# Performance work log

Measured on AMD Instinct MI355X. Metric: run time of the kernel, lower is better.

The kernel has to match this reference:

```python
import jax, jax.numpy as jnp
import numpy as np
import math

E, K = 8, 4
IN, OUT = 768, 768
B, S = 16, 512

def _nearest_factors(n):
    r = int(math.sqrt(n))
    while n % r != 0:
        r -= 1
    r = max(r, 1)
    return r, n // r

D1, D2 = _nearest_factors(IN)      # 24, 32
DO1, DO2 = _nearest_factors(OUT)   # 24, 32

def _cv_squared(v):
    v = v.astype(jnp.float32)
    return jnp.var(v, ddof=1) / (jnp.mean(v) ** 2 + 1e-10)

def setup_inputs() -> dict:
    key = jax.random.key(0)
    ks = jax.random.split(key, 8)
    eye = lambda d: jnp.broadcast_to(jnp.eye(d, dtype=jnp.float32), (E, d, d))
    return {
        "x": jax.random.normal(ks[0], (B, S, IN), jnp.float32),
        "w_gate": 0.02 * jax.random.normal(ks[1], (IN, E), jnp.float32),
        "weight": 0.02 * jax.random.normal(ks[2], (E, OUT, IN), jnp.float32),
        "res_weight": 0.02 * jax.random.normal(ks[3], (OUT, IN), jnp.float32),
        "curve1_in": eye(D1) + 0.01 * jax.random.normal(ks[4], (E, D1, D1), jnp.float32),
        "curve2_in": eye(D2) + 0.01 * jax.random.normal(ks[5], (E, D2, D2), jnp.float32),
        "curve1_out": eye(DO1) + 0.01 * jax.random.normal(ks[6], (E, DO1, DO1), jnp.float32),
        "curve2_out": eye(DO2) + 0.01 * jax.random.normal(ks[7], (E, DO2, DO2), jnp.float32),
    }

def reference(x, w_gate, weight, res_weight, curve1_in, curve2_in, curve1_out, curve2_out):
    b = x.shape[0]
    # ---- noisy_top_k_gating (eval mode: clean logits, no noise) ----
    xm = x.mean(-2)                         # [B, IN]
    logits = xm @ w_gate                    # [B, E]
    top_vals, top_idx = jax.lax.top_k(logits, min(K + 1, E))
    tk_vals = top_vals[:, :K]
    tk_idx = top_idx[:, :K]
    tk_gates = jax.nn.softmax(tk_vals, axis=1)
    gates = jnp.zeros_like(logits).at[jnp.arange(b)[:, None], tk_idx].set(tk_gates)
    load = (gates > 0).sum(0)               # eval: gates_to_load
    importance = gates.sum(0)
    loss = 0.01 * (_cv_squared(importance) + _cv_squared(load))
    # ---- curve-factor expert weight composition (k*2 >= n_experts branch) ----
    rtw = (weight - res_weight).reshape(E, DO1, DO2, D1, D2)
    rtw = jnp.einsum('bij,bjklm->biklm', curve1_out, rtw)
    rtw = jnp.einsum('bik,bjklm->bjilm', curve2_out, rtw)
    rtw = jnp.einsum('bil,bjklm->bjkim', curve1_in, rtw)
    rtw = jnp.einsum('bim,bjklm->bjkli', curve2_in, rtw)
    rtw = rtw.reshape(E, OUT, IN)
    # dropout p=0.1 is identity in eval mode
    expert_weights = res_weight + 0.9 * jnp.sum(rtw[None] * gates[:, :, None, None], axis=1)  # [B, OUT, IN]
    y = jnp.einsum('bsj,bkj->bsk', x, expert_weights)  # [B, S, OUT]
    return y, loss
```

## Files before the change

kernel.cpp:

```cpp
#include <hip/hip_runtime.h>
#include <hip/hip_bf16.h>

typedef unsigned short u16;
typedef __attribute__((ext_vector_type(8))) short bf16x8;
typedef __attribute__((ext_vector_type(4))) float f32x4;

#define NE 8
#define NTOPK 4
#define NIN 768
#define NOUT 768
#define NB 16
#define NS 512
#define YSZ (NB * NS * NOUT)
#define EWN (NOUT * NIN)

#define OFF_PART  0u
#define OFF_GATES 3145728u
#define OFF_XBF   3146240u
#define OFF_WD    15729152u
#define OFF_T1T   25166336u
#define OFF_RTW   34603520u
#define OFF_EW    44040704u

#define PRE_BAR(N) asm volatile("s_waitcnt vmcnt(" #N ")\n\ts_barrier" ::: "memory")
#define POST_BAR() asm volatile("s_waitcnt lgkmcnt(0)\n\ts_barrier" ::: "memory")

__device__ __forceinline__ u16 f2bf(float f) {
  union { float f; unsigned u; } v; v.f = f;
  unsigned r = v.u + 0x7fffu + ((v.u >> 16) & 1u);
  return (u16)(r >> 16);
}
__device__ __forceinline__ float bf2f(u16 h) {
  union { unsigned u; float f; } v; v.u = ((unsigned)h) << 16;
  return v.f;
}
__device__ __forceinline__ unsigned cvt2(float a, float b) {
  unsigned r;
  asm("v_cvt_pk_bf16_f32 %0, %1, %2" : "=v"(r) : "v"(a), "v"(b));
  return r;
}
__device__ __forceinline__ void gload16(const void* g, void* l) {
  __builtin_amdgcn_global_load_lds(
      (const __attribute__((address_space(1))) unsigned int*)g,
      (__attribute__((address_space(3))) unsigned int*)l, 16, 0, 0);
}
__device__ __forceinline__ void storeC(float* p, float v) { *p = v; }
__device__ __forceinline__ void storeC(u16* p, float v) { *p = f2bf(v); }

__global__ __launch_bounds__(256) void k_p0(const float* __restrict__ x,
                                            float* __restrict__ part,
                                            u16* __restrict__ xbf,
                                            const float* __restrict__ w,
                                            const float* __restrict__ res,
                                            u16* __restrict__ Wd) {
  int u = blockIdx.x;
  if (u < 1024) {
    int t = threadIdx.x;
    if (t < 192) {
      int b = u >> 6;
      int sc = u & 63;
      int c = t * 4;
      float a0 = 0.f, a1 = 0.f, a2 = 0.f, a3 = 0.f;
      int s0 = sc * 8;
#pragma unroll
      for (int r = 0; r < 8; ++r) {
        size_t ro = ((size_t)(b * NS + s0 + r)) * NIN;
        float4 v = *(const float4*)(x + ro + c);
        a0 += v.x; a1 += v.y; a2 += v.z; a3 += v.w;
        ushort4 o;
        o.x = f2bf(v.x); o.y = f2bf(v.y); o.z = f2bf(v.z); o.w = f2bf(v.w);
        *(ushort4*)(xbf + ro + c) = o;
      }
      float4 pv; pv.x = a0; pv.y = a1; pv.z = a2; pv.w = a3;
      *(float4*)(part + (size_t)(b * 64 + sc) * NIN + c) = pv;
    }
  } else {
    int b2 = u - 1024;
    int e = b2 / 288;
    int blk = b2 % 288;
    size_t base = (size_t)blk * 2048 + threadIdx.x * 8;
    float4 wa = *(const float4*)(w + (size_t)e * EWN + base);
    float4 wb = *(const float4*)(w + (size_t)e * EWN + base + 4);
    float4 ra = *(const float4*)(res + base);
    float4 rb = *(const float4*)(res + base + 4);
    bf16x8 o;
    o[0] = (short)f2bf(wa.x - ra.x); o[1] = (short)f2bf(wa.y - ra.y);
    o[2] = (short)f2bf(wa.z - ra.z); o[3] = (short)f2bf(wa.w - ra.w);
    o[4] = (short)f2bf(wb.x - rb.x); o[5] = (short)f2bf(wb.y - rb.y);
    o[6] = (short)f2bf(wb.z - rb.z); o[7] = (short)f2bf(wb.w - rb.w);
    *(bf16x8*)(Wd + (size_t)e * EWN + base) = o;
  }
}

__device__ __forceinline__ void body_logits(int b, float* red,
                                            const float* __restrict__ part,
                                            const float* __restrict__ w_gate,
                                            float* __restrict__ gates_out) {
  int tid = threadIdx.x;
  float p[NE] = {0.f, 0.f, 0.f, 0.f, 0.f, 0.f, 0.f, 0.f};
  for (int i = tid; i < NIN; i += 256) {
    float s = 0.f;
#pragma unroll
    for (int sc = 0; sc < 64; ++sc) s += part[(size_t)(b * 64 + sc) * NIN + i];
    float xmv = s * (1.0f / (float)NS);
#pragma unroll
    for (int e = 0; e < NE; ++e) p[e] += xmv * w_gate[i * NE + e];
  }
#pragma unroll
  for (int e = 0; e < NE; ++e) {
    float v = p[e];
    for (int off = 32; off; off >>= 1) v += __shfl_down(v, off);
    if ((tid & 63) == 0) red[(tid >> 6) * NE + e] = v;
  }
  __syncthreads();
  if (tid == 0) {
    float v[NE]; bool used[NE];
    for (int e = 0; e < NE; ++e) {
      v[e] = red[e] + red[NE + e] + red[2 * NE + e] + red[3 * NE + e];
      used[e] = false;
    }
    int idxs[NTOPK]; float vals[NTOPK];
    for (int t = 0; t < NTOPK; ++t) {
      int best = 0; float bv = -3.4e38f;
      for (int e = 0; e < NE; ++e)
        if (!used[e] && v[e] > bv) { bv = v[e]; best = e; }
      used[best] = true; idxs[t] = best; vals[t] = bv;
    }
    float m = vals[0];
    float ex[NTOPK]; float se = 0.f;
    for (int t = 0; t < NTOPK; ++t) { ex[t] = expf(vals[t] - m); se += ex[t]; }
    float g[NE];
    for (int e = 0; e < NE; ++e) g[e] = 0.f;
    for (int t = 0; t < NTOPK; ++t) g[idxs[t]] = ex[t] / se;
    for (int e = 0; e < NE; ++e) gates_out[b * NE + e] = g[e];
  }
}

__device__ __forceinline__ void body_kron(int bid, u16* lb,
                                          const float* __restrict__ c1,
                                          const float* __restrict__ c2,
                                          const u16* __restrict__ B,
                                          u16* __restrict__ C) {
  const int tid = threadIdx.x;
  const int lane = tid & 63;
  const int w = tid >> 6;
  const int wr = w >> 1, wc = w & 1;
  const int fr = lane & 15;
  const int kq = lane >> 4;
  const int swz = (bid & 7) * 72 + (bid >> 3);
  const int mb = swz % 12;
  const int nb = (swz / 12) % 6;
  const int e = swz / 72;
  const int m0 = mb * 64, n0 = nb * 128;
  const u16* Bb = B + (size_t)e * EWN;
  const float* c1b = c1 + e * 24 * 24;
  const float* c2b = c2 + e * 32 * 32;
  const int r1a = (m0 >> 5) + wr;
  float c2r[2][8];
  {
    const float* p0 = c2b + fr * 32 + kq * 8;
    const float* p1 = c2b + (16 + fr) * 32 + kq * 8;
#pragma unroll
    for (int j = 0; j < 8; ++j) { c2r[0][j] = p0[j]; c2r[1][j] = p1[j]; }
  }
  const int ob1 = (w * 2) * 1024 + lane * 16;
  const int ob2 = ob1 + 1024;
  const int rowB1 = ob1 >> 6, colB1 = ob1 & 63;
  const int rowB2 = ob2 >> 6, colB2 = ob2 & 63;

  auto STAGE = [&](int t) {
    int s = t & 3;
    int k0 = t * 32;
    gload16((const char*)Bb + ((size_t)(n0 + rowB1) * NIN + k0) * 2 + colB1,
            (char*)(lb + s * 4096) + ob1);
    gload16((const char*)Bb + ((size_t)(n0 + rowB2) * NIN + k0) * 2 + colB2,
            (char*)(lb + s * 4096) + ob2);
  };
  f32x4 acc[2][4] = {};
  auto COMPUTE = [&](int t) {
    int s = t & 3;
    const float ca = c1b[r1a * 24 + t];
    bf16x8 aF[2], bF[4];
#pragma unroll
    for (int m = 0; m < 2; ++m) {
      const float* cr = c2r[m];
      union { unsigned u[4]; bf16x8 v; } pk;
      pk.u[0] = cvt2(ca * cr[0], ca * cr[1]);
      pk.u[1] = cvt2(ca * cr[2], ca * cr[3]);
      pk.u[2] = cvt2(ca * cr[4], ca * cr[5]);
      pk.u[3] = cvt2(ca * cr[6], ca * cr[7]);
      aF[m] = pk.v;
    }
#pragma unroll
    for (int n = 0; n < 4; ++n)
      bF[n] = *(const bf16x8*)(lb + (size_t)s * 4096 + (wc * 64 + n * 16 + fr) * 32 + kq * 8);
#pragma unroll
    for (int m = 0; m < 2; ++m)
#pragma unroll
      for (int n = 0; n < 4; ++n)
        acc[m][n] = __builtin_amdgcn_mfma_f32_16x16x32_bf16(aF[m], bF[n], acc[m][n], 0, 0, 0);
  };

  STAGE(0); STAGE(1); STAGE(2); STAGE(3);
  for (int i = 0; i < 10; ++i) {
    PRE_BAR(4);
    COMPUTE(2 * i); COMPUTE(2 * i + 1);
    POST_BAR();
    STAGE(2 * i + 4); STAGE(2 * i + 5);
  }
  PRE_BAR(4);  COMPUTE(20); COMPUTE(21);  POST_BAR();
  PRE_BAR(0);  COMPUTE(22); COMPUTE(23);

  u16* Cb = C + (size_t)e * EWN;
#pragma unroll
  for (int m = 0; m < 2; ++m) {
    int rb = m0 + wr * 32 + m * 16 + kq * 4;
#pragma unroll
    for (int n = 0; n < 4; ++n) {
      int col = n0 + wc * 64 + n * 16 + fr;
#pragma unroll
      for (int r = 0; r < 4; ++r)
        storeC(Cb + (size_t)(rb + r) * NIN + col, acc[m][n][r]);
    }
  }
}

__global__ __launch_bounds__(256) void k_p1(const float* c1, const float* c2,
                                            const u16* B, u16* C,
                                            const float* part, const float* w_gate,
                                            float* gates) {
  __shared__ __attribute__((aligned(128))) u16 lB[4 * 128 * 32];
  __shared__ float red[NB * NE];
  if (blockIdx.x < 576) body_kron(blockIdx.x, lB, c1, c2, B, C);
  else                  body_logits(blockIdx.x - 576, red, part, w_gate, gates);
}
__global__ __launch_bounds__(256) void k_p2(const float* c1, const float* c2,
                                            const u16* B, u16* C) {
  __shared__ __attribute__((aligned(128))) u16 lB[4 * 128 * 32];
  body_kron(blockIdx.x, lB, c1, c2, B, C);
}

__global__ __launch_bounds__(256) void k_p3(const u16* __restrict__ rtwb,
                                            const float* __restrict__ res,
                                            const float* __restrict__ g,
                                            u16* __restrict__ ew,
                                            float* __restrict__ loss_out) {
  __shared__ float gsh[NB * NE];
  int bid = blockIdx.x;
  int tid = threadIdx.x;
  if (tid < NB * NE) gsh[tid] = 0.9f * g[tid];
  __syncthreads();
  if (bid == 0 && tid == 0) {
    float imp[NE], ld[NE];
    for (int e = 0; e < NE; ++e) {
      float si = 0.f, sl = 0.f;
      for (int b = 0; b < NB; ++b) {
        float gg = g[b * NE + e];
        si += gg; sl += (gg > 0.f) ? 1.f : 0.f;
      }
      imp[e] = si; ld[e] = sl;
    }
    float loss = 0.f;
    for (int which = 0; which < 2; ++which) {
      const float* a = which ? ld : imp;
      float mean = 0.f;
      for (int e = 0; e < NE; ++e) mean += a[e];
      mean *= (1.0f / NE);
      float var = 0.f;
      for (int e = 0; e < NE; ++e) { float d = a[e] - mean; var += d * d; }
      var *= (1.0f / (NE - 1));
      loss += var / (mean * mean + 1e-10f);
    }
    loss_out[0] = 0.01f * loss;
  }
  size_t base = ((size_t)bid * 256 + tid) * 8;
  float rv[NE][8];
#pragma unroll
  for (int e = 0; e < NE; ++e) {
    bf16x8 v = *(const bf16x8*)(rtwb + (size_t)e * EWN + base);
#pragma unroll
    for (int j = 0; j < 8; ++j) rv[e][j] = bf2f((u16)v[j]);
  }
  float r8[8];
  {
    float4 ra = *(const float4*)(res + base);
    float4 rb = *(const float4*)(res + base + 4);
    r8[0] = ra.x; r8[1] = ra.y; r8[2] = ra.z; r8[3] = ra.w;
    r8[4] = rb.x; r8[5] = rb.y; r8[6] = rb.z; r8[7] = rb.w;
  }
  for (int b = 0; b < NB; ++b) {
    float a[8];
#pragma unroll
    for (int j = 0; j < 8; ++j) a[j] = r8[j];
#pragma unroll
    for (int e = 0; e < NE; ++e) {
      float gg = gsh[b * NE + e];
#pragma unroll
      for (int j = 0; j < 8; ++j) a[j] += gg * rv[e][j];
    }
    bf16x8 o;
#pragma unroll
    for (int j = 0; j < 8; ++j) o[j] = (short)f2bf(a[j]);
    *(bf16x8*)(ew + (size_t)b * EWN + base) = o;
  }
}

__global__ __launch_bounds__(256) void k_main(const u16* __restrict__ A,
                                              const u16* __restrict__ Bw,
                                              float* __restrict__ C) {
  __shared__ __attribute__((aligned(128))) u16 la[3 * 128 * 32];
  __shared__ __attribute__((aligned(128))) u16 lb[3 * 128 * 32];
  const int tid = threadIdx.x;
  const int lane = tid & 63;
  const int w = tid >> 6;
  const int wr = w >> 1, wc = w & 1;
  const int fr = lane & 15;
  const int kq = lane >> 4;
  const int swz = (blockIdx.x & 7) * 48 + (blockIdx.x >> 3);
  const int mb = swz % 4;
  const int nb = (swz / 4) % 6;
  const int b = swz / 24;
  const int m0 = mb * 128, n0 = nb * 128;
  const u16* Ab = A + (size_t)b * NS * NIN;
  const u16* Bb = Bw + (size_t)b * EWN;
  const int ob1 = tid * 16;
  const int ob2 = ob1 + 4096;
  const int row1 = ob1 >> 6, col1 = ob1 & 63;
  const int row2 = ob2 >> 6, col2 = ob2 & 63;

  auto STAGE = [&](int t) {
    int s = t % 3;
    int k0 = t * 32;
    gload16((const char*)Ab + ((size_t)(m0 + row1) * NIN + k0) * 2 + col1,
            (char*)(la + s * 4096) + ob1);
    gload16((const char*)Ab + ((size_t)(m0 + row2) * NIN + k0) * 2 + col2,
            (char*)(la + s * 4096) + ob2);
    gload16((const char*)Bb + ((size_t)(n0 + row1) * NIN + k0) * 2 + col1,
            (char*)(lb + s * 4096) + ob1);
    gload16((const char*)Bb + ((size_t)(n0 + row2) * NIN + k0) * 2 + col2,
            (char*)(lb + s * 4096) + ob2);
  };
  f32x4 acc[4][4] = {};
  auto COMPUTE = [&](int t) {
    int s = t % 3;
    bf16x8 aF[4], bF[4];
#pragma unroll
    for (int m = 0; m < 4; ++m)
      aF[m] = *(const bf16x8*)(la + (size_t)s * 4096 + (wr * 64 + m * 16 + fr) * 32 + kq * 8);
#pragma unroll
    for (int n = 0; n < 4; ++n)
      bF[n] = *(const bf16x8*)(lb + (size_t)s * 4096 + (wc * 64 + n * 16 + fr) * 32 + kq * 8);
#pragma unroll
    for (int m = 0; m < 4; ++m)
#pragma unroll
      for (int n = 0; n < 4; ++n)
        acc[m][n] = __builtin_amdgcn_mfma_f32_16x16x32_bf16(aF[m], bF[n], acc[m][n], 0, 0, 0);
  };

  STAGE(0); STAGE(1); STAGE(2);
  for (int i = 0; i < 10; ++i) {
    PRE_BAR(4);
    COMPUTE(2 * i); COMPUTE(2 * i + 1);
    POST_BAR();
    STAGE(2 * i + 3); STAGE(2 * i + 4);
  }
  PRE_BAR(4);  COMPUTE(20); COMPUTE(21);  POST_BAR();
  STAGE(23);
  PRE_BAR(0);  COMPUTE(22); COMPUTE(23);

  float* Cb = C + (size_t)b * NS * NOUT;
#pragma unroll
  for (int m = 0; m < 4; ++m) {
    int rb = m0 + wr * 64 + m * 16 + kq * 4;
#pragma unroll
    for (int n = 0; n < 4; ++n) {
      int col = n0 + wc * 64 + n * 16 + fr;
#pragma unroll
      for (int r = 0; r < 4; ++r)
        Cb[(size_t)(rb + r) * NOUT + col] = acc[m][n][r];
    }
  }
}

extern "C" void kernel_launch(void* const* d_in, const int* in_sizes, int n_in,
                              void* d_out, int out_size, void* d_ws, size_t ws_size,
                              hipStream_t stream) {
  const float* x = (const float*)d_in[0];
  const float* w_gate = (const float*)d_in[1];
  const float* weight = (const float*)d_in[2];
  const float* res_w = (const float*)d_in[3];
  const float* c1i = (const float*)d_in[4];
  const float* c2i = (const float*)d_in[5];
  const float* c1o = (const float*)d_in[6];
  const float* c2o = (const float*)d_in[7];

  char* ws = (char*)d_ws;
  float* part = (float*)(ws + OFF_PART);
  float* gates = (float*)(ws + OFF_GATES);
  u16* xbf = (u16*)(ws + OFF_XBF);
  u16* Wd = (u16*)(ws + OFF_WD);
  u16* T1t = (u16*)(ws + OFF_T1T);
  u16* rtwb = (u16*)(ws + OFF_RTW);
  u16* ew = (u16*)(ws + OFF_EW);

  float* y = (float*)d_out;
  float* loss = y + YSZ;

  k_p0<<<dim3(3328), 256, 0, stream>>>(x, part, xbf, weight, res_w, Wd);
  k_p1<<<dim3(592), 256, 0, stream>>>(c1i, c2i, Wd, T1t, part, w_gate, gates);
  k_p2<<<dim3(576), 256, 0, stream>>>(c1o, c2o, T1t, rtwb);
  k_p3<<<dim3(288), 256, 0, stream>>>(rtwb, res_w, gates, ew, loss);
  k_main<<<dim3(384), 256, 0, stream>>>(xbf, ew, y);
}
```

Baseline: 76.37 us.

## Factor Kronecker curve transforms into separate small-mode contractions

Replaces the MFMA-based Kronecker GEMM, which multiplied each expert's 768x768 difference matrix by a dense 768x768 Kron(c1,c2) operand, with two separable scalar contractions: a 32x32 mode product (k_s1) followed by a 24x24 mode product (k_s2), each using LDS-cached factor matrices. The weight-minus-residual subtraction is fused into the first stage instead of running as its own pass. This cuts FLOPs substantially but drops tensor cores, adds two extra kernel launches, and round-trips a bf16 intermediate U through global memory, which adds another rounding step. The k_s2 reads are strided by 32*768, and k_s1 holds a per-thread 32-float register row.

```diff
diff --git a/kernel.cpp b/kernel.cpp
--- a/kernel.cpp
+++ b/kernel.cpp
@@ -17,7 +17,7 @@
 #define OFF_PART  0u
 #define OFF_GATES 3145728u
 #define OFF_XBF   3146240u
-#define OFF_WD    15729152u
+#define OFF_U     15729152u
 #define OFF_T1T   25166336u
 #define OFF_RTW   34603520u
 #define OFF_EW    44040704u
@@ -34,61 +34,34 @@
   union { unsigned u; float f; } v; v.u = ((unsigned)h) << 16;
   return v.f;
 }
-__device__ __forceinline__ unsigned cvt2(float a, float b) {
-  unsigned r;
-  asm("v_cvt_pk_bf16_f32 %0, %1, %2" : "=v"(r) : "v"(a), "v"(b));
-  return r;
-}
 __device__ __forceinline__ void gload16(const void* g, void* l) {
   __builtin_amdgcn_global_load_lds(
       (const __attribute__((address_space(1))) unsigned int*)g,
       (__attribute__((address_space(3))) unsigned int*)l, 16, 0, 0);
 }
-__device__ __forceinline__ void storeC(float* p, float v) { *p = v; }
-__device__ __forceinline__ void storeC(u16* p, float v) { *p = f2bf(v); }
-
-__global__ __launch_bounds__(256) void k_p0(const float* __restrict__ x,
-                                            float* __restrict__ part,
-                                            u16* __restrict__ xbf,
-                                            const float* __restrict__ w,
-                                            const float* __restrict__ res,
-                                            u16* __restrict__ Wd) {
+
+__global__ __launch_bounds__(256) void k_x(const float* __restrict__ x,
+                                           float* __restrict__ part,
+                                           u16* __restrict__ xbf) {
   int u = blockIdx.x;
-  if (u < 1024) {
-    int t = threadIdx.x;
-    if (t < 192) {
-      int b = u >> 6;
-      int sc = u & 63;
-      int c = t * 4;
-      float a0 = 0.f, a1 = 0.f, a2 = 0.f, a3 = 0.f;
-      int s0 = sc * 8;
-#pragma unroll
-      for (int r = 0; r < 8; ++r) {
-        size_t ro = ((size_t)(b * NS + s0 + r)) * NIN;
-        float4 v = *(const float4*)(x + ro + c);
-        a0 += v.x; a1 += v.y; a2 += v.z; a3 += v.w;
-        ushort4 o;
-        o.x = f2bf(v.x); o.y = f2bf(v.y); o.z = f2bf(v.z); o.w = f2bf(v.w);
-        *(ushort4*)(xbf + ro + c) = o;
-      }
-      float4 pv; pv.x = a0; pv.y = a1; pv.z = a2; pv.w = a3;
-      *(float4*)(part + (size_t)(b * 64 + sc) * NIN + c) = pv;
-    }
-  } else {
-    int b2 = u - 1024;
-    int e = b2 / 288;
-    int blk = b2 % 288;
-    size_t base = (size_t)blk * 2048 + threadIdx.x * 8;
-    float4 wa = *(const float4*)(w + (size_t)e * EWN + base);
-    float4 wb = *(const float4*)(w + (size_t)e * EWN + base + 4);
-    float4 ra = *(const float4*)(res + base);
-    float4 rb = *(const float4*)(res + base + 4);
-    bf16x8 o;
-    o[0] = (short)f2bf(wa.x - ra.x); o[1] = (short)f2bf(wa.y - ra.y);
-    o[2] = (short)f2bf(wa.z - ra.z); o[3] = (short)f2bf(wa.w - ra.w);
-    o[4] = (short)f2bf(wb.x - rb.x); o[5] = (short)f2bf(wb.y - rb.y);
-    o[6] = (short)f2bf(wb.z - rb.z); o[7] = (short)f2bf(wb.w - rb.w);
-    *(bf16x8*)(Wd + (size_t)e * EWN + base) = o;
+  int t = threadIdx.x;
+  if (t < 192) {
+    int b = u >> 6;
+    int sc = u & 63;
+    int c = t * 4;
+    float a0 = 0.f, a1 = 0.f, a2 = 0.f, a3 = 0.f;
+    int s0 = sc * 8;
+#pragma unroll
+    for (int r = 0; r < 8; ++r) {
+      size_t ro = ((size_t)(b * NS + s0 + r)) * NIN;
+      float4 v = *(const float4*)(x + ro + c);
+      a0 += v.x; a1 += v.y; a2 += v.z; a3 += v.w;
+      ushort4 o;
+      o.x = f2bf(v.x); o.y = f2bf(v.y); o.z = f2bf(v.z); o.w = f2bf(v.w);
+      *(ushort4*)(xbf + ro + c) = o;
+    }
+    float4 pv; pv.x = a0; pv.y = a1; pv.z = a2; pv.w = a3;
+    *(float4*)(part + (size_t)(b * 64 + sc) * NIN + c) = pv;
   }
 }
 
@@ -136,108 +109,78 @@
   }
 }
 
-__device__ __forceinline__ void body_kron(int bid, u16* lb,
-                                          const float* __restrict__ c1,
-                                          const float* __restrict__ c2,
-                                          const u16* __restrict__ B,
-                                          u16* __restrict__ C) {
-  const int tid = threadIdx.x;
-  const int lane = tid & 63;
-  const int w = tid >> 6;
-  const int wr = w >> 1, wc = w & 1;
-  const int fr = lane & 15;
-  const int kq = lane >> 4;
-  const int swz = (bid & 7) * 72 + (bid >> 3);
-  const int mb = swz % 12;
-  const int nb = (swz / 12) % 6;
-  const int e = swz / 72;
-  const int m0 = mb * 64, n0 = nb * 128;
-  const u16* Bb = B + (size_t)e * EWN;
-  const float* c1b = c1 + e * 24 * 24;
-  const float* c2b = c2 + e * 32 * 32;
-  const int r1a = (m0 >> 5) + wr;
-  float c2r[2][8];
-  {
-    const float* p0 = c2b + fr * 32 + kq * 8;
-    const float* p1 = c2b + (16 + fr) * 32 + kq * 8;
-#pragma unroll
-    for (int j = 0; j < 8; ++j) { c2r[0][j] = p0[j]; c2r[1][j] = p1[j]; }
-  }
-  const int ob1 = (w * 2) * 1024 + lane * 16;
-  const int ob2 = ob1 + 1024;
-  const int rowB1 = ob1 >> 6, colB1 = ob1 & 63;
-  const int rowB2 = ob2 >> 6, colB2 = ob2 & 63;
-
-  auto STAGE = [&](int t) {
-    int s = t & 3;
-    int k0 = t * 32;
-    gload16((const char*)Bb + ((size_t)(n0 + rowB1) * NIN + k0) * 2 + colB1,
-            (char*)(lb + s * 4096) + ob1);
-    gload16((const char*)Bb + ((size_t)(n0 + rowB2) * NIN + k0) * 2 + colB2,
-            (char*)(lb + s * 4096) + ob2);
-  };
-  f32x4 acc[2][4] = {};
-  auto COMPUTE = [&](int t) {
-    int s = t & 3;
-    const float ca = c1b[r1a * 24 + t];
-    bf16x8 aF[2], bF[4];
-#pragma unroll
-    for (int m = 0; m < 2; ++m) {
-      const float* cr = c2r[m];
-      union { unsigned u[4]; bf16x8 v; } pk;
-      pk.u[0] = cvt2(ca * cr[0], ca * cr[1]);
-      pk.u[1] = cvt2(ca * cr[2], ca * cr[3]);
-      pk.u[2] = cvt2(ca * cr[4], ca * cr[5]);
-      pk.u[3] = cvt2(ca * cr[6], ca * cr[7]);
-      aF[m] = pk.v;
-    }
-#pragma unroll
-    for (int n = 0; n < 4; ++n)
-      bF[n] = *(const bf16x8*)(lb + (size_t)s * 4096 + (wc * 64 + n * 16 + fr) * 32 + kq * 8);
-#pragma unroll
-    for (int m = 0; m < 2; ++m)
-#pragma unroll
-      for (int n = 0; n < 4; ++n)
-        acc[m][n] = __builtin_amdgcn_mfma_f32_16x16x32_bf16(aF[m], bF[n], acc[m][n], 0, 0, 0);
-  };
-
-  STAGE(0); STAGE(1); STAGE(2); STAGE(3);
-  for (int i = 0; i < 10; ++i) {
-    PRE_BAR(4);
-    COMPUTE(2 * i); COMPUTE(2 * i + 1);
-    POST_BAR();
-    STAGE(2 * i + 4); STAGE(2 * i + 5);
-  }
-  PRE_BAR(4);  COMPUTE(20); COMPUTE(21);  POST_BAR();
-  PRE_BAR(0);  COMPUTE(22); COMPUTE(23);
-
-  u16* Cb = C + (size_t)e * EWN;
-#pragma unroll
-  for (int m = 0; m < 2; ++m) {
-    int rb = m0 + wr * 32 + m * 16 + kq * 4;
-#pragma unroll
-    for (int n = 0; n < 4; ++n) {
-      int col = n0 + wc * 64 + n * 16 + fr;
-#pragma unroll
-      for (int r = 0; r < 4; ++r)
-        storeC(Cb + (size_t)(rb + r) * NIN + col, acc[m][n][r]);
-    }
-  }
-}
-
-__global__ __launch_bounds__(256) void k_p1(const float* c1, const float* c2,
-                                            const u16* B, u16* C,
-                                            const float* part, const float* w_gate,
-                                            float* gates) {
-  __shared__ __attribute__((aligned(128))) u16 lB[4 * 128 * 32];
+template <bool WSUB>
+__global__ __launch_bounds__(256) void k_s1(const float* __restrict__ wsrc,
+                                            const float* __restrict__ res,
+                                            const u16* __restrict__ tin,
+                                            const float* __restrict__ c2,
+                                            u16* __restrict__ U,
+                                            const float* __restrict__ part,
+                                            const float* __restrict__ w_gate,
+                                            float* __restrict__ gates) {
+  __shared__ float c2lds[32 * 32];
   __shared__ float red[NB * NE];
-  if (blockIdx.x < 576) body_kron(blockIdx.x, lB, c1, c2, B, C);
-  else                  body_logits(blockIdx.x - 576, red, part, w_gate, gates);
-}
-__global__ __launch_bounds__(256) void k_p2(const float* c1, const float* c2,
-                                            const u16* B, u16* C) {
-  __shared__ __attribute__((aligned(128))) u16 lB[4 * 128 * 32];
-  body_kron(blockIdx.x, lB, c1, c2, B, C);
+  int bid = blockIdx.x;
+  if (bid >= 576) {
+    if (gates) body_logits(bid - 576, red, part, w_gate, gates);
+    return;
+  }
+  int e = bid / 72, rem = bid % 72, l = rem / 3, chunk = rem % 3;
+  int jk = chunk * 256 + threadIdx.x;
+  for (int idx = threadIdx.x; idx < 1024; idx += 256) c2lds[idx] = c2[e * 1024 + idx];
+  __syncthreads();
+  float wr[32];
+  if (WSUB) {
+    const float* wp = wsrc + ((size_t)(e * NIN + jk)) * NIN + l * 32;
+    const float* rp = res + (size_t)jk * NIN + l * 32;
+#pragma unroll
+    for (int q = 0; q < 8; ++q) {
+      float4 a = *(const float4*)(wp + q * 4);
+      float4 b = *(const float4*)(rp + q * 4);
+      wr[q * 4 + 0] = a.x - b.x; wr[q * 4 + 1] = a.y - b.y;
+      wr[q * 4 + 2] = a.z - b.z; wr[q * 4 + 3] = a.w - b.w;
+    }
+  } else {
+    const u16* tp = tin + ((size_t)(e * NIN + jk)) * NIN + l * 32;
+#pragma unroll
+    for (int q = 0; q < 4; ++q) {
+      bf16x8 v = *(const bf16x8*)(tp + q * 8);
+#pragma unroll
+      for (int j = 0; j < 8; ++j) wr[q * 8 + j] = bf2f((u16)v[j]);
+    }
+  }
+  size_t ubase = ((size_t)(e * 24 + l) * 32) * 768 + jk;
+#pragma unroll 4
+  for (int i2 = 0; i2 < 32; ++i2) {
+    float acc = 0.f;
+#pragma unroll
+    for (int m = 0; m < 32; ++m) acc += c2lds[i2 * 32 + m] * wr[m];
+    U[ubase + (size_t)i2 * 768] = f2bf(acc);
+  }
+}
+
+__global__ __launch_bounds__(256) void k_s2(const u16* __restrict__ U,
+                                            const float* __restrict__ c1,
+                                            u16* __restrict__ out) {
+  __shared__ float c1lds[24 * 24];
+  int bid = blockIdx.x;
+  int e = bid / 96, rem = bid % 96, r2 = rem / 3, chunk = rem % 3;
+  int col = chunk * 256 + threadIdx.x;
+  for (int idx = threadIdx.x; idx < 576; idx += 256) c1lds[idx] = c1[e * 576 + idx];
+  __syncthreads();
+  float acc[24];
+#pragma unroll
+  for (int i1 = 0; i1 < 24; ++i1) acc[i1] = 0.f;
+  size_t ubase = ((size_t)(e * 24) * 32 + r2) * 768 + col;
+#pragma unroll 4
+  for (int l = 0; l < 24; ++l) {
+    float u = bf2f(U[ubase + (size_t)l * 32 * 768]);
+#pragma unroll
+    for (int i1 = 0; i1 < 24; ++i1) acc[i1] += c1lds[i1 * 24 + l] * u;
+  }
+#pragma unroll 4
+  for (int i1 = 0; i1 < 24; ++i1)
+    out[((size_t)(e * NIN + i1 * 32 + r2)) * NIN + col] = f2bf(acc[i1]);
 }
 
 __global__ __launch_bounds__(256) void k_p3(const u16* __restrict__ rtwb,
@@ -398,7 +341,7 @@
   float* part = (float*)(ws + OFF_PART);
   float* gates = (float*)(ws + OFF_GATES);
   u16* xbf = (u16*)(ws + OFF_XBF);
-  u16* Wd = (u16*)(ws + OFF_WD);
+  u16* U = (u16*)(ws + OFF_U);
   u16* T1t = (u16*)(ws + OFF_T1T);
   u16* rtwb = (u16*)(ws + OFF_RTW);
   u16* ew = (u16*)(ws + OFF_EW);
@@ -406,9 +349,11 @@
   float* y = (float*)d_out;
   float* loss = y + YSZ;
 
-  k_p0<<<dim3(3328), 256, 0, stream>>>(x, part, xbf, weight, res_w, Wd);
-  k_p1<<<dim3(592), 256, 0, stream>>>(c1i, c2i, Wd, T1t, part, w_gate, gates);
-  k_p2<<<dim3(576), 256, 0, stream>>>(c1o, c2o, T1t, rtwb);
+  k_x<<<dim3(1024), 256, 0, stream>>>(x, part, xbf);
+  k_s1<true><<<dim3(592), 256, 0, stream>>>(weight, res_w, nullptr, c2i, U, part, w_gate, gates);
+  k_s2<<<dim3(768), 256, 0, stream>>>(U, c1i, T1t);
+  k_s1<false><<<dim3(576), 256, 0, stream>>>(nullptr, nullptr, T1t, c2o, U, nullptr, nullptr, nullptr);
+  k_s2<<<dim3(768), 256, 0, stream>>>(U, c1o, rtwb);
   k_p3<<<dim3(288), 256, 0, stream>>>(rtwb, res_w, gates, ew, loss);
   k_main<<<dim3(384), 256, 0, stream>>>(xbf, ew, y);
 }
```

Measured after the change: 97.01 us. 1.27x slower.
